# Performance work log

Hardware: AMD Instinct MI355X
Metric: run time of the kernel (lower is better)

Reference implementation:

```python
import jax, jax.numpy as jnp
import numpy as np
from jax import lax

B, N = 16, 8192          # batch, points per cloud
G, K = 512, 32           # num_groups, group_size
TOKEN_DIM = 384
BN_EPS = 1e-5


def setup_inputs() -> dict:
    key = jax.random.key(0)
    ks = jax.random.split(key, 8)
    w = lambda i, shape: jax.random.normal(ks[i], shape, jnp.float32) * 0.05
    return {
        "points": jax.random.normal(ks[0], (B, N, 3), jnp.float32),
        # first_conv: Conv1d(3,128,1,bias=False) -> BN(128) -> ReLU -> Conv1d(128,256,1)
        "w1": w(1, (128, 3)),
        "bn1_gamma": jnp.ones((128,), jnp.float32),
        "bn1_beta": jnp.zeros((128,), jnp.float32),
        "bn1_mean": jnp.zeros((128,), jnp.float32),
        "bn1_var": jnp.ones((128,), jnp.float32),
        "w2": w(2, (256, 128)),
        "b2": jnp.zeros((256,), jnp.float32),
        # second_conv: Conv1d(512,512,1,bias=False) -> BN(512) -> ReLU -> Conv1d(512,384,1)
        "w3": w(3, (512, 512)),
        "bn2_gamma": jnp.ones((512,), jnp.float32),
        "bn2_beta": jnp.zeros((512,), jnp.float32),
        "bn2_mean": jnp.zeros((512,), jnp.float32),
        "bn2_var": jnp.ones((512,), jnp.float32),
        "w4": w(4, (TOKEN_DIM, 512)),
        "b4": jnp.zeros((TOKEN_DIM,), jnp.float32),
    }


def _fps(xyz, num_samples):
    """Farthest point sampling. xyz: [B,N,3] -> idx [B,num_samples] (start = point 0)."""
    b, n, _ = xyz.shape
    start = jnp.zeros((b,), jnp.int32)
    init_min = jnp.full((b, n), 1e10, xyz.dtype)

    def body(carry, _):
        min_d2, last = carry
        last_pt = jnp.take_along_axis(xyz, last[:, None, None], axis=1)  # [B,1,3]
        d2 = jnp.sum((xyz - last_pt) ** 2, axis=-1)                      # [B,N]
        min_d2 = jnp.minimum(min_d2, d2)
        nxt = jnp.argmax(min_d2, axis=-1).astype(jnp.int32)
        return (min_d2, nxt), last

    _, idx = lax.scan(body, (init_min, start), None, length=num_samples)
    return idx.T  # [B,num_samples]


def _bn(x, gamma, beta, mean, var):
    # inference batchnorm over last (channel) axis
    return (x - mean) * lax.rsqrt(var + BN_EPS) * gamma + beta


def reference(points, w1, bn1_gamma, bn1_beta, bn1_mean, bn1_var, w2, b2,
              w3, bn2_gamma, bn2_beta, bn2_mean, bn2_var, w4, b4):
    xyz = points[:, :, :3]
    fidx = _fps(xyz, G)                                       # [B,G]
    centers = jnp.take_along_axis(xyz, fidx[:, :, None], 1)   # [B,G,3]

    # brute-force KNN via squared distances [B,G,N]
    pn = jnp.sum(xyz * xyz, -1)                               # [B,N]
    cn = jnp.sum(centers * centers, -1)                       # [B,G]
    d2 = cn[:, :, None] + pn[:, None, :] - 2.0 * jnp.einsum('bgc,bnc->bgn', centers, xyz)
    _, idx = lax.top_k(-d2, K)                                # [B,G,K] nearest indices

    groups = jax.vmap(lambda p, i: p[i])(points, idx)          # [B,G,K,3]
    groups = groups - centers[:, :, None, :]                   # center-relative coords

    x = groups.reshape(B * G, K, 3)                            # [M,K,3]
    # first_conv
    f = jnp.einsum('mkc,dc->mkd', x, w1)                       # [M,K,128]
    f = jax.nn.relu(_bn(f, bn1_gamma, bn1_beta, bn1_mean, bn1_var))
    f = jnp.einsum('mkd,ed->mke', f, w2) + b2                  # [M,K,256]
    g = jnp.max(f, axis=1, keepdims=True)                      # [M,1,256]
    f = jnp.concatenate([jnp.broadcast_to(g, f.shape), f], -1) # [M,K,512]
    # second_conv
    f = jnp.einsum('mke,fe->mkf', f, w3)                       # [M,K,512]
    f = jax.nn.relu(_bn(f, bn2_gamma, bn2_beta, bn2_mean, bn2_var))
    f = jnp.einsum('mkf,of->mko', f, w4) + b4                  # [M,K,384]
    tokens = jnp.max(f, axis=1).reshape(B, G, TOKEN_DIM)
    return tokens, centers
```

## Files before the change

kernel.cpp:

```cpp
#include <hip/hip_runtime.h>
#include <stdint.h>

#define PB 16
#define PN 8192
#define PG 512
#define PK 32
#define PTOK 384
#define PM (PB*PG)
#define PMK (PM*PK)
#define NWORK 240
#define NTASK (PM/4)
static constexpr float BN_EPS_C = 1e-5f;

typedef short bh8  __attribute__((ext_vector_type(8)));
typedef float f32x4 __attribute__((ext_vector_type(4)));

__device__ __forceinline__ short f2bf(float f){
  unsigned u = __float_as_uint(f);
  unsigned r = u + 0x7fffu + ((u>>16)&1u);
  return (short)(r>>16);
}
__device__ __forceinline__ float bf2f(short s){
  return __uint_as_float(((unsigned)(unsigned short)s)<<16);
}
__device__ __forceinline__ void gload16(const void* g, void* l){
  __builtin_amdgcn_global_load_lds((const __attribute__((address_space(1))) unsigned int*)g,
                                   (__attribute__((address_space(3))) unsigned int*)l,
                                   16, 0, 0);
}

__global__ __launch_bounds__(1024, 4) void mega2_kernel(
    const float* __restrict__ points, float* __restrict__ centers,
    int* __restrict__ prog, int* __restrict__ qhead,
    float* __restrict__ grp){
#pragma clang fp contract(off)
  __shared__ __align__(16) char SMEM[150528];
  const int t = threadIdx.x;
  const int lane = t & 63;

  if (blockIdx.x < PB){
    const int b = blockIdx.x;
    const float* P = points + (size_t)b*PN*3;
    float4* Lc = (float4*)SMEM;
    unsigned short* sidx = (unsigned short*)(SMEM + 131072);
    int* shist = (int*)(SMEM + 147456);
    int* spart = (int*)(SMEM + 149504);
    unsigned long long* swa = (unsigned long long*)(SMEM + 149760);
    if (t < 512) shist[t] = 0;
    if (t < 3)   swa[t] = 0ull;
    __syncthreads();
    int mycell[8];
#pragma unroll
    for (int i=0;i<8;i++){
      int j = i*1024 + t;
      float x=P[j*3+0], y=P[j*3+1], z=P[j*3+2];
      Lc[j] = make_float4(x,y,z,0.f);
      int qx=(int)fminf(fmaxf((x+4.f)*1.0f,0.f),7.f);
      int qy=(int)fminf(fmaxf((y+4.f)*1.0f,0.f),7.f);
      int qz=(int)fminf(fmaxf((z+4.f)*1.0f,0.f),7.f);
      int mc = (qx&1)|((qx&2)<<2)|((qx&4)<<4)
             | ((qy&1)<<1)|((qy&2)<<3)|((qy&4)<<5)
             | ((qz&1)<<2)|((qz&2)<<4)|((qz&4)<<6);
      mycell[i]=mc;
      atomicAdd(&shist[mc],1);
    }
    __syncthreads();
    if (t < 64){
      int acc=0;
#pragma unroll
      for (int k=0;k<8;k++){ int h=shist[t*8+k]; shist[t*8+k]=acc; acc+=h; }
      spart[t]=acc;
    }
    __syncthreads();
    if (t==0){ int acc=0; for (int k=0;k<64;k++){ int h=spart[k]; spart[k]=acc; acc+=h; } }
    __syncthreads();
    if (t < 64){
      int off=spart[t];
#pragma unroll
      for (int k=0;k<8;k++) shist[t*8+k] += off;
    }
    __syncthreads();
#pragma unroll
    for (int i=0;i<8;i++){
      int j = i*1024 + t;
      int r = atomicAdd(&shist[mycell[i]],1);
      sidx[r] = (unsigned short)j;
    }
    __syncthreads();
    float px[8],py[8],pz[8],md[8]; int lowc[8];
    float tlx=1e30f,tly=1e30f,tlz=1e30f,thx=-1e30f,thy=-1e30f,thz=-1e30f;
#pragma unroll
    for (int i=0;i<8;i++){
      int oj = sidx[t*8+i];
      float4 p4 = Lc[oj];
      float x=p4.x, y=p4.y, z=p4.z;
      px[i]=x; py[i]=y; pz[i]=z; md[i]=1e10f; lowc[i]=PN-1-oj;
      tlx=fminf(tlx,x); thx=fmaxf(thx,x);
      tly=fminf(tly,y); thy=fmaxf(thy,y);
      tlz=fminf(tlz,z); thz=fmaxf(thz,z);
    }
#pragma unroll
    for (int off=32; off; off>>=1){
      tlx=fminf(tlx,__shfl_xor(tlx,off)); thx=fmaxf(thx,__shfl_xor(thx,off));
      tly=fminf(tly,__shfl_xor(tly,off)); thy=fmaxf(thy,__shfl_xor(thy,off));
      tlz=fminf(tlz,__shfl_xor(tlz,off)); thz=fmaxf(thz,__shfl_xor(thz,off));
    }
    unsigned long long wkey = ((unsigned long long)0x7F800000u)<<32;
    float cx=P[0], cy=P[1], cz=P[2];
    if (t==0){ float* c = centers + (size_t)b*PG*3; c[0]=cx; c[1]=cy; c[2]=cz; }
    __syncthreads();
    for (int g=1; g<PG; g++){
      const int sl = g%3, ns = (g+1)%3;
      float ddx=fmaxf(fmaxf(tlx-cx, cx-thx),0.f);
      float ddy=fmaxf(fmaxf(tly-cy, cy-thy),0.f);
      float ddz=fmaxf(fmaxf(tlz-cz, cz-thz),0.f);
      float dmin2=((ddx*ddx+ddy*ddy)+ddz*ddz)*0.999999f;
      if (!(dmin2 >= __uint_as_float((unsigned)(wkey>>32)))){
        unsigned long long bk = 0ull;
#pragma unroll
        for (int i=0;i<8;i++){
          float dx=px[i]-cx, dy=py[i]-cy, dz=pz[i]-cz;
          float d2 = (dx*dx + dy*dy) + dz*dz;
          md[i] = fminf(md[i], d2);
          unsigned long long ki = ((unsigned long long)__float_as_uint(md[i])<<32)
                                | (unsigned)lowc[i];
          if (ki > bk) bk = ki;
        }
#pragma unroll
        for (int mask=32; mask; mask>>=1){
          unsigned long long o = __shfl_xor(bk, mask);
          if (o > bk) bk = o;
        }
        wkey = bk;
      }
      if (lane==0) atomicMax(&swa[sl], wkey);
      if (t==0) swa[ns] = 0ull;
      __syncthreads();
      unsigned long long w = swa[sl];
      int j = PN-1 - (int)(w & 0xFFFFFFFFu);
      float4 c4 = Lc[j];
      cx = c4.x; cy = c4.y; cz = c4.z;
      if (t==0){
        float* cc = centers + ((size_t)b*PG + g)*3;
        cc[0]=cx; cc[1]=cy; cc[2]=cz;
        if ((g & 3) == 3)
          __hip_atomic_store(prog + b, g + 1, __ATOMIC_RELEASE, __HIP_MEMORY_SCOPE_AGENT);
      }
    }
  }

  unsigned long long* ks_k = (unsigned long long*)(SMEM + 149504);
  int*   ks_idx = (int*)(SMEM + 149760);
  float* ks_c   = (float*)(SMEM + 150272);
  int*   s_task = (int*)(SMEM + 150320);

  for(;;){
    if (t == 0){
      int id = atomicAdd(qhead, 1);
      s_task[0] = id;
      if (id < NTASK){
        int bb = id & (PB-1), qq = id >> 4;
        int need = qq*4 + 4;
        while (__hip_atomic_load(prog + bb, __ATOMIC_ACQUIRE, __HIP_MEMORY_SCOPE_AGENT) < need)
          __builtin_amdgcn_s_sleep(10);
      }
    }
    __syncthreads();
    const int id = s_task[0];
    if (id >= NTASK) break;
    const int b = id & (PB-1), q = id >> 4;
    const int m0 = b*PG + q*4;
    const float* P = points + (size_t)b*PN*3;
    const int sub = t >> 8, tt = t & 255;

    if (tt == 0){
      const float* cp = centers + (size_t)(m0 + sub)*3;
      ks_c[sub*3+0] = __hip_atomic_load(cp+0, __ATOMIC_ACQUIRE, __HIP_MEMORY_SCOPE_AGENT);
      ks_c[sub*3+1] = __hip_atomic_load(cp+1, __ATOMIC_ACQUIRE, __HIP_MEMORY_SCOPE_AGENT);
      ks_c[sub*3+2] = __hip_atomic_load(cp+2, __ATOMIC_ACQUIRE, __HIP_MEMORY_SCOPE_AGENT);
    }
    __syncthreads();
    {
      const float cx=ks_c[sub*3+0], cy=ks_c[sub*3+1], cz=ks_c[sub*3+2];
      const float cn = (cx*cx + cy*cy) + cz*cz;
      unsigned key[PK];
#pragma unroll
      for (int i=0;i<PK;i++){
        int j = i*256 + tt;
        float x=P[j*3+0], y=P[j*3+1], z=P[j*3+2];
        float pn = (x*x + y*y) + z*z;
        float e  = (cx*x + cy*y) + cz*z;
        float d2 = (cn + pn) - 2.0f*e;
        unsigned u = __float_as_uint(d2);
        u ^= (u & 0x80000000u) ? 0xFFFFFFFFu : 0x80000000u;
        key[i] = u;
      }
      unsigned lmin = key[0]; int li = 0;
#pragma unroll
      for (int i=1;i<PK;i++) if (key[i] < lmin){ lmin = key[i]; li = i; }
      unsigned long long lkey = ((unsigned long long)lmin << 32)
                              | (unsigned)(li*256 + tt);
      const int widx = tt >> 6;
      for (int it=0; it<PK; it++){
        unsigned long long v = lkey;
#pragma unroll
        for (int off=32; off; off>>=1){
          unsigned long long o = __shfl_down(v, off);
          if (o < v) v = o;
        }
        if (lane==0) ks_k[sub*8 + (it&1)*4 + widx] = v;
        __syncthreads();
        unsigned long long w = ks_k[sub*8 + (it&1)*4 + 0];
#pragma unroll
        for (int qq=1;qq<4;qq++){
          unsigned long long o = ks_k[sub*8 + (it&1)*4 + qq];
          if (o < w) w = o;
        }
        int wj = (int)(w & 0xFFFFFFFFull);
        if (tt==0) ks_idx[sub*32 + it] = wj;
        if ((wj & 255) == tt){
          key[wj >> 8] = 0xFFFFFFFFu;
          lmin = key[0]; li = 0;
#pragma unroll
          for (int i=1;i<PK;i++) if (key[i] < lmin){ lmin = key[i]; li = i; }
          lkey = ((unsigned long long)lmin << 32) | (unsigned)(li*256 + tt);
        }
      }
      __syncthreads();
      if (tt < PK*3){
        int k = tt/3, c = tt - k*3;
        int j = ks_idx[sub*32 + k];
        grp[((size_t)(m0 + sub)*PK + k)*3 + c] = P[j*3+c] - ks_c[sub*3+c];
      }
    }
  }
}

__global__ __launch_bounds__(512, 2) void mlp_kernel(const float* __restrict__ grp,
                                                     const float* __restrict__ w1,
                                                     const float* __restrict__ sc1,
                                                     const float* __restrict__ sh1,
                                                     const short* __restrict__ w2b,
                                                     const float* __restrict__ b2,
                                                     const short* __restrict__ w3ab,
                                                     const short* __restrict__ w3bb,
                                                     const float* __restrict__ sc2,
                                                     const float* __restrict__ sh2,
                                                     const short* __restrict__ w4b,
                                                     const float* __restrict__ b4,
                                                     float* __restrict__ tokens){
  __shared__ __align__(16) short s_f1f3[16384];
  __shared__ __align__(16) short s_f2[32768];
  __shared__ __align__(16) short s_g[1024];
  __shared__ __align__(16) short s_bst[24576];
  const int t = threadIdx.x;
  const int lane = t & 63, wid = t >> 6;
  const int mh = wid >> 1, nq = wid & 1;
  const int B0 = blockIdx.x * 128;
  const int G0 = blockIdx.x * 4;
  const int srow = lane >> 2;
  const int scol = (lane & 3) * 8;
  const int frow = lane & 15;
  const int fk   = (lane >> 4) * 8;
  const int rb   = (lane >> 4) * 4;
  const int cb   = lane & 15;

  {
    int r = t & 127, dg = t >> 7;
    float x0 = grp[(size_t)(B0+r)*3 + 0];
    float x1 = grp[(size_t)(B0+r)*3 + 1];
    float x2 = grp[(size_t)(B0+r)*3 + 2];
#pragma unroll
    for (int dd=0; dd<32; dd++){
      int d = dg*32 + dd;
      float a = x0*w1[d*3+0] + x1*w1[d*3+1] + x2*w1[d*3+2];
      float y = a*sc1[d] + sh1[d];
      s_f1f3[dg*4096 + r*32 + dd] = f2bf(fmaxf(y, 0.f));
    }
  }
  __syncthreads();

  {
    f32x4 accB[2][8] = {};
    for (int k0=0; k0<128; k0+=64){
      for (int cc=wid; cc<32; cc+=8){
        int sub = cc & 1, rc = cc >> 1;
        int r = rc*16 + srow;
        gload16(w2b + (size_t)r*128 + k0 + sub*32 + scol, &s_bst[sub*8192 + rc*512]);
      }
      __syncthreads();
#pragma unroll
      for (int sub=0; sub<2; sub++){
        int kc = (k0 + sub*32) >> 5;
        bh8 af[2], bf[8];
#pragma unroll
        for (int i=0;i<2;i++)
          af[i] = *(const bh8*)&s_f1f3[kc*4096 + (mh*32 + i*16 + frow)*32 + fk];
#pragma unroll
        for (int j=0;j<8;j++)
          bf[j] = *(const bh8*)&s_bst[sub*8192 + (nq*128 + j*16 + frow)*32 + fk];
#pragma unroll
        for (int i=0;i<2;i++)
#pragma unroll
          for (int j=0;j<8;j++)
            accB[i][j] = __builtin_amdgcn_mfma_f32_16x16x32_bf16(af[i], bf[j], accB[i][j], 0,0,0);
      }
      __syncthreads();
    }
#pragma unroll
    for (int i=0;i<2;i++)
#pragma unroll
      for (int j=0;j<8;j++){
        int col = nq*128 + j*16 + cb;
#pragma unroll
        for (int r=0;r<4;r++){
          int row = mh*32 + i*16 + rb + r;
          s_f2[(col>>5)*4096 + row*32 + (col&31)] = f2bf(accB[i][j][r] + b2[col]);
        }
      }
  }
  __syncthreads();

  {
#pragma unroll
    for (int task=0; task<2; task++){
      int g = (t>>8) + task*2;
      int col = t & 255;
      int kc = col >> 5, c5 = col & 31;
      float mx = -3.4e38f;
#pragma unroll
      for (int kk=0; kk<PK; kk++)
        mx = fmaxf(mx, bf2f(s_f2[kc*4096 + (g*32 + kk)*32 + c5]));
      s_g[g*256 + col] = f2bf(mx);
    }
  }
  __syncthreads();

  f32x4 acc4[2][12] = {};
  for (int nc=0; nc<4; nc++){
    f32x4 acc3[2][4] = {};
    for (int k0=0; k0<512; k0+=64){
      const short* w3s = (k0 < 256) ? w3ab : w3bb;
      int kk0 = (k0 < 256) ? k0 : (k0 - 256);
      for (int cc=wid; cc<16; cc+=8){
        int sub = cc & 1, rc = cc >> 1;
        int r = nc*128 + rc*16 + srow;
        gload16(w3s + (size_t)r*256 + kk0 + sub*32 + scol, &s_bst[sub*4096 + rc*512]);
      }
      __syncthreads();
#pragma unroll
      for (int sub=0; sub<2; sub++){
        int k = k0 + sub*32;
        bh8 af[2], bf[4];
        if (k < 256){
#pragma unroll
          for (int i=0;i<2;i++)
            af[i] = *(const bh8*)&s_g[mh*256 + k + fk];
        } else {
          int kc = (k - 256) >> 5;
#pragma unroll
          for (int i=0;i<2;i++)
            af[i] = *(const bh8*)&s_f2[kc*4096 + (mh*32 + i*16 + frow)*32 + fk];
        }
#pragma unroll
        for (int j=0;j<4;j++)
          bf[j] = *(const bh8*)&s_bst[sub*4096 + (nq*64 + j*16 + frow)*32 + fk];
#pragma unroll
        for (int i=0;i<2;i++)
#pragma unroll
          for (int j=0;j<4;j++)
            acc3[i][j] = __builtin_amdgcn_mfma_f32_16x16x32_bf16(af[i], bf[j], acc3[i][j], 0,0,0);
      }
      __syncthreads();
    }
#pragma unroll
    for (int i=0;i<2;i++)
#pragma unroll
      for (int j=0;j<4;j++){
        int cl = nq*64 + j*16 + cb;
        int f  = nc*128 + cl;
        float s = sc2[f], h = sh2[f];
#pragma unroll
        for (int r=0;r<4;r++){
          int row = mh*32 + i*16 + rb + r;
          float v = acc3[i][j][r]*s + h;
          s_f1f3[(cl>>5)*4096 + row*32 + (cl&31)] = f2bf(fmaxf(v, 0.f));
        }
      }
    __syncthreads();
    for (int kk0=0; kk0<128; kk0+=64){
      for (int cc=wid; cc<48; cc+=8){
        int sub = cc & 1, rc = cc >> 1;
        int r = rc*16 + srow;
        gload16(w4b + (size_t)r*512 + nc*128 + kk0 + sub*32 + scol, &s_bst[sub*12288 + rc*512]);
      }
      __syncthreads();
#pragma unroll
      for (int sub=0; sub<2; sub++){
        int kc = (kk0 + sub*32) >> 5;
        bh8 af[2], bf[12];
#pragma unroll
        for (int i=0;i<2;i++)
          af[i] = *(const bh8*)&s_f1f3[kc*4096 + (mh*32 + i*16 + frow)*32 + fk];
#pragma unroll
        for (int j=0;j<12;j++)
          bf[j] = *(const bh8*)&s_bst[sub*12288 + (nq*192 + j*16 + frow)*32 + fk];
#pragma unroll
        for (int i=0;i<2;i++)
#pragma unroll
          for (int j=0;j<12;j++)
            acc4[i][j] = __builtin_amdgcn_mfma_f32_16x16x32_bf16(af[i], bf[j], acc4[i][j], 0,0,0);
      }
      __syncthreads();
    }
  }

#pragma unroll
  for (int j=0;j<12;j++){
    int col = nq*192 + j*16 + cb;
    float mx = -3.4e38f;
#pragma unroll
    for (int i=0;i<2;i++)
#pragma unroll
      for (int r=0;r<4;r++)
        mx = fmaxf(mx, acc4[i][j][r]);
    mx = fmaxf(mx, __shfl_xor(mx, 16));
    mx = fmaxf(mx, __shfl_xor(mx, 32));
    if (lane < 16)
      tokens[(size_t)(G0 + mh)*PTOK + col] = mx + b4[col];
  }
}

__global__ __launch_bounds__(256) void prep_kernel(const float* __restrict__ w2,
    const float* __restrict__ w3, const float* __restrict__ w4,
    const float* __restrict__ g1, const float* __restrict__ be1,
    const float* __restrict__ mu1, const float* __restrict__ va1,
    const float* __restrict__ g2, const float* __restrict__ be2,
    const float* __restrict__ mu2, const float* __restrict__ va2,
    short* __restrict__ w2b, short* __restrict__ w3ab, short* __restrict__ w3bb,
    short* __restrict__ w4b, float* __restrict__ sc1, float* __restrict__ sh1,
    float* __restrict__ sc2, float* __restrict__ sh2,
    int* __restrict__ prog, int* __restrict__ qhead){
  int i = blockIdx.x*256 + threadIdx.x;
  if (i < 256*128) w2b[i] = f2bf(w2[i]);
  if (i < 512*512){
    int f = i >> 9, e = i & 511;
    short v = f2bf(w3[i]);
    if (e < 256) w3ab[f*256 + e] = v; else w3bb[f*256 + (e-256)] = v;
  }
  if (i < 384*512) w4b[i] = f2bf(w4[i]);
  if (i < 128){ float s = g1[i]*rsqrtf(va1[i] + BN_EPS_C); sc1[i]=s; sh1[i]=be1[i]-mu1[i]*s; }
  if (i < 512){ float s = g2[i]*rsqrtf(va2[i] + BN_EPS_C); sc2[i]=s; sh2[i]=be2[i]-mu2[i]*s; }
  if (i < PB) prog[i] = 0;
  if (i == PB) qhead[0] = 0;
}

extern "C" void kernel_launch(void* const* d_in, const int* in_sizes, int n_in,
                              void* d_out, int out_size, void* d_ws, size_t ws_size,
                              hipStream_t stream){
  const float* points = (const float*)d_in[0];
  const float* w1  = (const float*)d_in[1];
  const float* g1  = (const float*)d_in[2];
  const float* be1 = (const float*)d_in[3];
  const float* mu1 = (const float*)d_in[4];
  const float* va1 = (const float*)d_in[5];
  const float* w2  = (const float*)d_in[6];
  const float* b2  = (const float*)d_in[7];
  const float* w3  = (const float*)d_in[8];
  const float* g2  = (const float*)d_in[9];
  const float* be2 = (const float*)d_in[10];
  const float* mu2 = (const float*)d_in[11];
  const float* va2 = (const float*)d_in[12];
  const float* w4  = (const float*)d_in[13];
  const float* b4  = (const float*)d_in[14];
  float* tokens  = (float*)d_out;
  float* centers = (float*)d_out + (size_t)PM*PTOK;

  char* ws = (char*)d_ws;
  float* grp  = (float*)(ws + 0);
  short* w2b  = (short*)(ws + 3145728ull);
  short* w3ab = (short*)(ws + 3211264ull);
  short* w3bb = (short*)(ws + 3473408ull);
  short* w4b  = (short*)(ws + 3735552ull);
  float* sc1  = (float*)(ws + 4128768ull);
  float* sh1  = (float*)(ws + 4129280ull);
  float* sc2  = (float*)(ws + 4129792ull);
  float* sh2  = (float*)(ws + 4131840ull);
  int*   prog = (int*)(ws + 4133888ull);
  int*   qhead= (int*)(ws + 4133952ull);

  prep_kernel<<<1024, 256, 0, stream>>>(w2, w3, w4, g1, be1, mu1, va1, g2, be2, mu2, va2,
                                        w2b, w3ab, w3bb, w4b, sc1, sh1, sc2, sh2,
                                        prog, qhead);
  mega2_kernel<<<PB + NWORK, 1024, 0, stream>>>(points, centers, prog, qhead, grp);
  mlp_kernel<<<PMK/128, 512, 0, stream>>>(grp, w1, sc1, sh1, w2b, b2,
                                          w3ab, w3bb, sc2, sh2, w4b, b4, tokens);
}
```

Baseline: 1.049 ms.

## Replace iterative kNN argmin loop with two-pass radix histogram select and bitonic sort

Replaces the 32-iteration block-wide argmin extraction for top-K nearest neighbours with a two-level radix select. Key histograms over the top 16 bits find the threshold bucket, survivors are compacted into shared memory, and a 64-wide wave bitonic sort orders them. The original iterative path stays as a fallback when more than 64 candidates survive. This removes 32 rounds of shuffle reductions and block barriers per group, at the cost of shared-memory atomics on histograms. Shared-memory offsets for scratch are relocated to the start of SMEM.

Result: no change. 1.062 ms (+1.2%).

```diff
diff --git a/kernel.cpp b/kernel.cpp
--- a/kernel.cpp
+++ b/kernel.cpp
@@ -149,10 +149,15 @@
     }
   }
 
+  unsigned* s_hist = (unsigned*)SMEM;
+  unsigned long long* s_surv = (unsigned long long*)(SMEM + 4096);
+  int*   s_sct   = (int*)(SMEM + 6144);
+  int*   s_bparm = (int*)(SMEM + 6160);
+  int*   s_flag  = (int*)(SMEM + 6192);
+  float* ks_c    = (float*)(SMEM + 6208);
+  int*   s_task  = (int*)(SMEM + 6256);
   unsigned long long* ks_k = (unsigned long long*)(SMEM + 149504);
-  int*   ks_idx = (int*)(SMEM + 149760);
-  float* ks_c   = (float*)(SMEM + 150272);
-  int*   s_task = (int*)(SMEM + 150320);
+  int*   ks_idx  = (int*)(SMEM + 149760);
 
   for(;;){
     if (t == 0){
@@ -172,7 +177,11 @@
     const int m0 = b*PG + q*4;
     const float* P = points + (size_t)b*PN*3;
     const int sub = t >> 8, tt = t & 255;
-
+    const int swv = tt >> 6;
+
+    s_hist[t] = 0;
+    if (t < 4)  s_sct[t] = 0;
+    if (t == 0) s_flag[0] = 0;
     if (tt == 0){
       const float* cp = centers + (size_t)(m0 + sub)*3;
       ks_c[sub*3+0] = __hip_atomic_load(cp+0, __ATOMIC_ACQUIRE, __HIP_MEMORY_SCOPE_AGENT);
@@ -180,21 +189,145 @@
       ks_c[sub*3+2] = __hip_atomic_load(cp+2, __ATOMIC_ACQUIRE, __HIP_MEMORY_SCOPE_AGENT);
     }
     __syncthreads();
-    {
-      const float cx=ks_c[sub*3+0], cy=ks_c[sub*3+1], cz=ks_c[sub*3+2];
-      const float cn = (cx*cx + cy*cy) + cz*cz;
-      unsigned key[PK];
+
+    const float cx=ks_c[sub*3+0], cy=ks_c[sub*3+1], cz=ks_c[sub*3+2];
+    const float cn = (cx*cx + cy*cy) + cz*cz;
+    unsigned key[PK];
+#pragma unroll
+    for (int i=0;i<PK;i++){
+      int j = i*256 + tt;
+      float x=P[j*3+0], y=P[j*3+1], z=P[j*3+2];
+      float pn = (x*x + y*y) + z*z;
+      float e  = (cx*x + cy*y) + cz*z;
+      float d2 = (cn + pn) - 2.0f*e;
+      unsigned u = __float_as_uint(d2);
+      u ^= (u & 0x80000000u) ? 0xFFFFFFFFu : 0x80000000u;
+      key[i] = u;
+      atomicAdd(&s_hist[sub*256 + (u>>24)], 1u);
+    }
+    __syncthreads();
+
+    int B = 0, nless = 0;
+    if (swv == 0){
+      unsigned v0 = s_hist[sub*256 + lane*4 + 0];
+      unsigned v1 = s_hist[sub*256 + lane*4 + 1];
+      unsigned v2 = s_hist[sub*256 + lane*4 + 2];
+      unsigned v3 = s_hist[sub*256 + lane*4 + 3];
+      unsigned tot = ((v0 + v1) + v2) + v3;
+      unsigned inc = tot;
+      for (int off=1; off<64; off<<=1){
+        unsigned n = __shfl_up(inc, off);
+        if (lane >= off) inc += n;
+      }
+      unsigned excl = inc - tot;
+      unsigned c0 = excl + v0, c1 = c0 + v1, c2 = c1 + v2, c3 = c2 + v3;
+      int cand = 1<<30;
+      if (c3 >= 32u){
+        cand = lane*4 + 3;
+        if (c2 >= 32u) cand = lane*4 + 2;
+        if (c1 >= 32u) cand = lane*4 + 1;
+        if (c0 >= 32u) cand = lane*4 + 0;
+      }
+      int Bc = cand;
+      for (int m=32; m; m>>=1){ int o = __shfl_xor(Bc, m); if (o < Bc) Bc = o; }
+      int src = Bc >> 2, kk = Bc & 3;
+      unsigned cc01 = (c0 & 0xFFFFu) | (c1 << 16);
+      unsigned cc23 = (c2 & 0xFFFFu) | (c3 << 16);
+      unsigned vv01 = (v0 & 0xFFFFu) | (v1 << 16);
+      unsigned vv23 = (v2 & 0xFFFFu) | (v3 << 16);
+      unsigned a01 = __shfl(cc01, src), a23 = __shfl(cc23, src);
+      unsigned w01 = __shfl(vv01, src), w23 = __shfl(vv23, src);
+      unsigned Sincl = (kk==0) ? (a01 & 0xFFFFu) : (kk==1) ? (a01 >> 16)
+                     : (kk==2) ? (a23 & 0xFFFFu) : (a23 >> 16);
+      unsigned vB    = (kk==0) ? (w01 & 0xFFFFu) : (kk==1) ? (w01 >> 16)
+                     : (kk==2) ? (w23 & 0xFFFFu) : (w23 >> 16);
+      B = Bc; nless = (int)(Sincl - vB);
+      if (tt == 0) s_bparm[sub*2+0] = B;
+    }
+    __syncthreads();
+    B = s_bparm[sub*2+0];
+    s_hist[t] = 0;
+    __syncthreads();
+
+#pragma unroll
+    for (int i=0;i<PK;i++){
+      unsigned u = key[i];
+      if ((int)(u>>24) == B) atomicAdd(&s_hist[sub*256 + ((u>>16)&255u)], 1u);
+    }
+    __syncthreads();
+
+    if (swv == 0){
+      unsigned v0 = s_hist[sub*256 + lane*4 + 0];
+      unsigned v1 = s_hist[sub*256 + lane*4 + 1];
+      unsigned v2 = s_hist[sub*256 + lane*4 + 2];
+      unsigned v3 = s_hist[sub*256 + lane*4 + 3];
+      unsigned tot = ((v0 + v1) + v2) + v3;
+      unsigned inc = tot;
+      for (int off=1; off<64; off<<=1){
+        unsigned n = __shfl_up(inc, off);
+        if (lane >= off) inc += n;
+      }
+      unsigned excl = inc - tot;
+      unsigned c0 = excl + v0, c1 = c0 + v1, c2 = c1 + v2, c3 = c2 + v3;
+      unsigned thr = 32u - (unsigned)nless;
+      int cand = 1<<30;
+      if (c3 >= thr){
+        cand = lane*4 + 3;
+        if (c2 >= thr) cand = lane*4 + 2;
+        if (c1 >= thr) cand = lane*4 + 1;
+        if (c0 >= thr) cand = lane*4 + 0;
+      }
+      int Bc = cand;
+      for (int m=32; m; m>>=1){ int o = __shfl_xor(Bc, m); if (o < Bc) Bc = o; }
+      int src = Bc >> 2, kk = Bc & 3;
+      unsigned cc01 = (c0 & 0xFFFFu) | (c1 << 16);
+      unsigned cc23 = (c2 & 0xFFFFu) | (c3 << 16);
+      unsigned a01 = __shfl(cc01, src), a23 = __shfl(cc23, src);
+      unsigned Sincl = (kk==0) ? (a01 & 0xFFFFu) : (kk==1) ? (a01 >> 16)
+                     : (kk==2) ? (a23 & 0xFFFFu) : (a23 >> 16);
+      int S2 = nless + (int)Sincl;
+      if (tt == 0){
+        s_bparm[sub*2+1] = Bc;
+        if (S2 > 64) s_flag[0] = 1;
+      }
+    }
+    if (swv == 1) s_surv[sub*64 + lane] = ~0ull;
+    __syncthreads();
+    const int B2 = s_bparm[sub*2+1];
+    const int doFB = s_flag[0];
+
+    if (!doFB){
 #pragma unroll
       for (int i=0;i<PK;i++){
-        int j = i*256 + tt;
-        float x=P[j*3+0], y=P[j*3+1], z=P[j*3+2];
-        float pn = (x*x + y*y) + z*z;
-        float e  = (cx*x + cy*y) + cz*z;
-        float d2 = (cn + pn) - 2.0f*e;
-        unsigned u = __float_as_uint(d2);
-        u ^= (u & 0x80000000u) ? 0xFFFFFFFFu : 0x80000000u;
-        key[i] = u;
-      }
+        unsigned u = key[i];
+        int hb = (int)(u >> 24), b2v = (int)((u >> 16) & 255u);
+        if (hb < B || (hb == B && b2v <= B2)){
+          int ix = atomicAdd(&s_sct[sub], 1);
+          if (ix < 64)
+            s_surv[sub*64 + ix] = ((unsigned long long)u << 32) | (unsigned)(i*256 + tt);
+        }
+      }
+    }
+    __syncthreads();
+    if (!doFB){
+      if (swv == 0){
+        unsigned long long v = s_surv[sub*64 + lane];
+        for (int k=2; k<=64; k<<=1)
+          for (int j2=k>>1; j2>=1; j2>>=1){
+            unsigned long long o = __shfl_xor(v, j2);
+            bool keepMin = (((lane & j2) == 0) == ((lane & k) == 0));
+            unsigned long long mn = (v < o) ? v : o;
+            unsigned long long mx = (v < o) ? o : v;
+            v = keepMin ? mn : mx;
+          }
+        if (lane < PK){
+          int j = (int)(v & 0xFFFFFFFFull);
+#pragma unroll
+          for (int c=0;c<3;c++)
+            grp[((size_t)(m0+sub)*PK + lane)*3 + c] = P[j*3+c] - ks_c[sub*3+c];
+        }
+      }
+    } else {
       unsigned lmin = key[0]; int li = 0;
 #pragma unroll
       for (int i=1;i<PK;i++) if (key[i] < lmin){ lmin = key[i]; li = i; }
@@ -219,7 +352,9 @@
         int wj = (int)(w & 0xFFFFFFFFull);
         if (tt==0) ks_idx[sub*32 + it] = wj;
         if ((wj & 255) == tt){
-          key[wj >> 8] = 0xFFFFFFFFu;
+          int slot = wj >> 8;
+#pragma unroll
+          for (int i=0;i<PK;i++) if (i == slot) key[i] = 0xFFFFFFFFu;
           lmin = key[0]; li = 0;
 #pragma unroll
           for (int i=1;i<PK;i++) if (key[i] < lmin){ lmin = key[i]; li = i; }
```
